# Performance work log

Hardware: AMD Instinct MI355X
Metric: run time of the kernel (lower is better)

## Reference

```python
import jax, jax.numpy as jnp
import numpy as np

B, T, C, D = 8, 4096, 1024, 128  # batch, seq (=block_size), dim_embd, head_features

def setup_inputs() -> dict:
    key = jax.random.key(0)
    k1, k2, k3, k4 = jax.random.split(key, 4)
    s = 0.02
    return {
        "x": jax.random.normal(k1, (B, T, C), dtype=jnp.float32),
        "wq": jax.random.normal(k2, (C, D), dtype=jnp.float32) * s,
        "wk": jax.random.normal(k3, (C, D), dtype=jnp.float32) * s,
        "wv": jax.random.normal(k4, (C, D), dtype=jnp.float32) * s,
    }

def reference(x, wq, wk, wv):
    # q,k,v: [B,T,D]
    q = jnp.einsum('btc,cd->btd', x, wq)
    k = jnp.einsum('btc,cd->btd', x, wk)
    v = jnp.einsum('btc,cd->btd', x, wv)
    scale = k.shape[-1] ** -0.5
    wei = jnp.einsum('bqd,bkd->bqk', q, k) * scale  # [B,T,T]
    causal = jnp.tril(jnp.ones((T, T), dtype=bool))
    wei = jnp.where(causal, wei, -jnp.inf)
    attn = jax.nn.softmax(wei, axis=-1)  # dropout p=0.0 -> identity
    out = jnp.einsum('bqk,bkd->bqd', attn, v)  # [B,T,D]
    return out
```

## Files before the change

### kernel.cpp

```cpp
#include <hip/hip_runtime.h>

#define TT 4096
#define CC 1024
#define DD 128

typedef __attribute__((ext_vector_type(8))) short s16x8;
typedef __attribute__((ext_vector_type(4))) short s16x4;
typedef __attribute__((ext_vector_type(8))) __bf16 bf16x8;
typedef __attribute__((ext_vector_type(4))) float f32x4;

__device__ __forceinline__ short f2bf(float f) {
    union { float f; unsigned u; } v; v.f = f;
    unsigned r = v.u + 0x7fffu + ((v.u >> 16) & 1u);
    return (short)(r >> 16);
}

__device__ __forceinline__ unsigned cvt_pk(float lo, float hi) {
    unsigned r;
    asm("v_cvt_pk_bf16_f32 %0, %1, %2" : "=v"(r) : "v"(lo), "v"(hi));
    return r;
}

__device__ __forceinline__ f32x4 mfma16(s16x8 a, s16x8 b, f32x4 c) {
    return __builtin_amdgcn_mfma_f32_16x16x32_bf16(
        __builtin_bit_cast(bf16x8, a), __builtin_bit_cast(bf16x8, b), c, 0, 0, 0);
}

__device__ __forceinline__ void gload_lds16(const short* g, short* l) {
    __builtin_amdgcn_global_load_lds(
        (const __attribute__((address_space(1))) void*)g,
        (__attribute__((address_space(3))) void*)l, 16, 0, 0);
}

__global__ void wt_kernel(const float* __restrict__ wq, const float* __restrict__ wk,
                          const float* __restrict__ wv, short* __restrict__ wT) {
    int idx = blockIdx.x * 256 + threadIdx.x;
    int d = idx & 127;
    int c = (idx >> 7) & 1023;
    int wsel = idx >> 17;
    const float* w = (wsel == 0) ? wq : (wsel == 1) ? wk : wv;
    float v = w[(size_t)c * DD + d];
    if (wsel == 0) v *= 0.08838834764831845f;
    wT[(size_t)wsel * DD * CC + (size_t)d * CC + c] = f2bf(v);
}

__global__ __launch_bounds__(512)
void qkv_kernel(const float* __restrict__ x, const short* __restrict__ wT,
                short* __restrict__ qo, short* __restrict__ ko, short* __restrict__ vTo) {
    __shared__ short lw[2][384 * 64];
    const int mt = blockIdx.x;
    const int tid = threadIdx.x, lane = tid & 63, wid = tid >> 6;
    const int l15 = lane & 15, g = lane >> 4;
    const int wm = wid >> 1, wn = wid & 1;
    const int arow = mt * 128 + wm * 32 + l15;
    const float* xr0 = x + (size_t)arow * CC + g * 8;
    const float* xr1 = xr0 + (size_t)16 * CC;

    const f32x4 fz = {0.f, 0.f, 0.f, 0.f};
    f32x4 acc[2][12];
#pragma unroll
    for (int mr = 0; mr < 2; mr++)
#pragma unroll
        for (int nr = 0; nr < 12; nr++) acc[mr][nr] = fz;

    const int swr = wid * 48;
    const short* wsrc = wT + (size_t)(swr + (lane >> 3)) * CC + (lane & 7) * 8;

    float4 pa[2][2][2];
#define LOADA(kc) do { \
    _Pragma("unroll") for (int mr_ = 0; mr_ < 2; mr_++) \
    _Pragma("unroll") for (int ks_ = 0; ks_ < 2; ks_++) { \
        const float* p_ = (mr_ ? xr1 : xr0) + (kc) * 64 + ks_ * 32; \
        pa[mr_][ks_][0] = *(const float4*)p_; \
        pa[mr_][ks_][1] = *(const float4*)(p_ + 4); } \
} while (0)
#define STAGEW(kc, buf) do { \
    _Pragma("unroll") for (int j_ = 0; j_ < 6; j_++) \
        gload_lds16(wsrc + (size_t)(j_ * 8) * CC + (kc) * 64, &lw[buf][(swr + j_ * 8) * 64]); \
} while (0)

    LOADA(0);
    STAGEW(0, 0);
    asm volatile("s_waitcnt vmcnt(0)" ::: "memory");
    __builtin_amdgcn_s_barrier();
    int cur = 0;

    for (int kc = 0; kc < 16; kc++) {
        s16x8 af[2][2];
#pragma unroll
        for (int mr = 0; mr < 2; mr++)
#pragma unroll
            for (int ks = 0; ks < 2; ks++) {
                union { unsigned u[4]; s16x8 v; } cv;
                cv.u[0] = cvt_pk(pa[mr][ks][0].x, pa[mr][ks][0].y);
                cv.u[1] = cvt_pk(pa[mr][ks][0].z, pa[mr][ks][0].w);
                cv.u[2] = cvt_pk(pa[mr][ks][1].x, pa[mr][ks][1].y);
                cv.u[3] = cvt_pk(pa[mr][ks][1].z, pa[mr][ks][1].w);
                af[mr][ks] = cv.v;
            }
        if (kc < 15) { LOADA(kc + 1); STAGEW(kc + 1, cur ^ 1); }
        __builtin_amdgcn_s_setprio(1);
#pragma unroll
        for (int ks = 0; ks < 2; ks++)
#pragma unroll
            for (int nr = 0; nr < 12; nr++) {
                const s16x8 bfg = *(const s16x8*)
                    &lw[cur][(wn * 192 + nr * 16 + l15) * 64 + ks * 32 + g * 8];
                acc[0][nr] = mfma16(af[0][ks], bfg, acc[0][nr]);
                acc[1][nr] = mfma16(af[1][ks], bfg, acc[1][nr]);
            }
        __builtin_amdgcn_s_setprio(0);
        asm volatile("s_waitcnt vmcnt(0) lgkmcnt(0)" ::: "memory");
        __builtin_amdgcn_s_barrier();
        cur ^= 1;
    }

    const int bidx = mt >> 5;
    const int tb = (mt & 31) * 128 + wm * 32;
#pragma unroll
    for (int mr = 0; mr < 2; mr++)
#pragma unroll
        for (int nr = 0; nr < 12; nr++) {
            const int n = wn * 192 + nr * 16 + l15;
            if (n < 256) {
                short* dst; int d;
                if (n < 128) { dst = qo; d = n; } else { dst = ko; d = n - 128; }
#pragma unroll
                for (int i = 0; i < 4; i++) {
                    int t = tb + mr * 16 + g * 4 + i;
                    dst[((size_t)bidx * TT + t) * DD + d] = f2bf(acc[mr][nr][i]);
                }
            } else {
                const int d = n - 256;
                const int t = tb + mr * 16 + g * 4;
                uint2 u;
                u.x = cvt_pk(acc[mr][nr][0], acc[mr][nr][1]);
                u.y = cvt_pk(acc[mr][nr][2], acc[mr][nr][3]);
                *(uint2*)(vTo + ((size_t)bidx * DD + d) * TT + t) = u;
            }
        }
}

__device__ __forceinline__ void attn_stage8(const short* kT, const short* vT, int kv0,
                                            short* lkb, short* lvb, int wid, int lane) {
#pragma unroll
    for (int j = 0; j < 2; j++) {
        int rbk = wid * 8 + j * 4;
        int rk = rbk + (lane >> 4);
        int ck = (lane & 15) ^ (rk & 7);
        gload_lds16(kT + (size_t)(kv0 + rk) * DD + ck * 8, lkb + rbk * 128);
        int rbv = wid * 16 + j * 8;
        int dv = rbv + (lane >> 3);
        int cv = (lane & 7) ^ (dv & 7);
        gload_lds16(vT + (size_t)dv * TT + kv0 + cv * 8, lvb + rbv * 64);
    }
}

__global__ __launch_bounds__(512)
void attn_kernel(const short* __restrict__ qb, const short* __restrict__ kb,
                 const short* __restrict__ vb, float* __restrict__ out) {
    __shared__ short lk[2][64 * 128];
    __shared__ short lv[2][128 * 64];
    __shared__ short lp[8 * 16 * 64];
    const int id = blockIdx.x;
    const int b = id & 7;
    const int p = id >> 3;
    const int tid = threadIdx.x, lane = tid & 63, wid = tid >> 6;
    const int l15 = lane & 15, g = lane >> 4;
    const int qt_w = (wid < 4) ? p : 63 - p;
    const int wq0 = qt_w * 64 + (wid & 3) * 16;
    const int tmax = 63 - p;

    s16x8 qf[4];
    {
        const short* qp = qb + ((size_t)b * TT + wq0 + l15) * DD + g * 8;
#pragma unroll
        for (int ks = 0; ks < 4; ks++) qf[ks] = *(const s16x8*)(qp + ks * 32);
    }
    const f32x4 fz = {0.f, 0.f, 0.f, 0.f};
    f32x4 o[8];
#pragma unroll
    for (int n = 0; n < 8; n++) o[n] = fz;
    float rmax = -1e30f, rsum = 0.f;

    const short* kT = kb + (size_t)b * TT * DD;
    const short* vT = vb + (size_t)b * DD * TT;

    attn_stage8(kT, vT, 0, lk[0], lv[0], wid, lane);
    asm volatile("s_waitcnt vmcnt(0)" ::: "memory");
    __builtin_amdgcn_s_barrier();
    int cur = 0;

    for (int t = 0; t <= tmax; t++) {
        if (t < tmax) attn_stage8(kT, vT, (t + 1) * 64, lk[cur ^ 1], lv[cur ^ 1], wid, lane);
        if (t <= qt_w) {
            const int kv0 = t * 64;
            const char* lkc = (const char*)&lk[cur][0];
            const char* lvc = (const char*)&lv[cur][0];

            f32x4 s[4];
            __builtin_amdgcn_s_setprio(1);
#pragma unroll
            for (int sub = 0; sub < 4; sub++) {
                f32x4 a = fz;
#pragma unroll
                for (int ks = 0; ks < 4; ks++) {
                    int row = sub * 16 + l15;
                    int byte = (row * 256 + ks * 64 + g * 16) ^ ((row & 7) << 4);
                    s16x8 kf = *(const s16x8*)(lkc + byte);
                    a = mfma16(kf, qf[ks], a);
                }
                s[sub] = a;
            }
            __builtin_amdgcn_s_setprio(0);
            if (t == qt_w) {
#pragma unroll
                for (int sub = 0; sub < 4; sub++)
#pragma unroll
                    for (int i = 0; i < 4; i++) {
                        int k = kv0 + sub * 16 + 4 * g + i;
                        if (k > wq0 + l15) s[sub][i] = -1e30f;
                    }
            }
            float m0 = s[0][0];
#pragma unroll
            for (int sub = 0; sub < 4; sub++)
#pragma unroll
                for (int i = 0; i < 4; i++) m0 = fmaxf(m0, s[sub][i]);
            m0 = fmaxf(m0, __shfl_xor(m0, 16));
            m0 = fmaxf(m0, __shfl_xor(m0, 32));
            float mnew = fmaxf(rmax, m0);
            float scal = __expf(rmax - mnew);
            rmax = mnew;
            float ls = 0.f;
#pragma unroll
            for (int sub = 0; sub < 4; sub++)
#pragma unroll
                for (int i = 0; i < 4; i++) {
                    float pv = __expf(s[sub][i] - mnew);
                    s[sub][i] = pv;
                    ls += pv;
                }
            ls += __shfl_xor(ls, 16);
            ls += __shfl_xor(ls, 32);
            rsum = rsum * scal + ls;
#pragma unroll
            for (int sub = 0; sub < 4; sub++) {
                uint2 w01;
                w01.x = cvt_pk(s[sub][0], s[sub][1]);
                w01.y = cvt_pk(s[sub][2], s[sub][3]);
                int byte = (l15 * 128 + sub * 32 + g * 8) ^ ((l15 & 7) << 4);
                *(uint2*)((char*)lp + wid * 2048 + byte) = w01;
            }
#pragma unroll
            for (int n = 0; n < 8; n++)
#pragma unroll
                for (int i = 0; i < 4; i++) o[n][i] *= scal;
            __builtin_amdgcn_s_setprio(1);
#pragma unroll
            for (int ks2 = 0; ks2 < 2; ks2++) {
                int pbyte = (l15 * 128 + ks2 * 64 + g * 16) ^ ((l15 & 7) << 4);
                s16x8 pf = *(const s16x8*)((const char*)lp + wid * 2048 + pbyte);
#pragma unroll
                for (int n = 0; n < 8; n++) {
                    int vrow = n * 16 + l15;
                    int vbyte = (vrow * 128 + ks2 * 64 + g * 16) ^ ((vrow & 7) << 4);
                    s16x8 vf = *(const s16x8*)(lvc + vbyte);
                    o[n] = mfma16(vf, pf, o[n]);
                }
            }
            __builtin_amdgcn_s_setprio(0);
        }
        asm volatile("s_waitcnt vmcnt(0) lgkmcnt(0)" ::: "memory");
        __builtin_amdgcn_s_barrier();
        cur ^= 1;
    }
    float inv = 1.0f / rsum;
    float* orow = out + ((size_t)b * TT + wq0 + l15) * DD;
#pragma unroll
    for (int n = 0; n < 8; n++) {
        float4 r;
        r.x = o[n][0] * inv; r.y = o[n][1] * inv;
        r.z = o[n][2] * inv; r.w = o[n][3] * inv;
        *(float4*)(orow + n * 16 + 4 * g) = r;
    }
}

extern "C" void kernel_launch(void* const* d_in, const int* in_sizes, int n_in,
                              void* d_out, int out_size, void* d_ws, size_t ws_size,
                              hipStream_t stream) {
    const float* x  = (const float*)d_in[0];
    const float* wq = (const float*)d_in[1];
    const float* wk = (const float*)d_in[2];
    const float* wv = (const float*)d_in[3];
    float* out = (float*)d_out;
    char* ws = (char*)d_ws;
    short* wT = (short*)ws;
    short* qb = (short*)(ws + 786432);
    short* kb = (short*)(ws + 786432 + 8388608);
    short* vb = (short*)(ws + 786432 + 16777216);

    wt_kernel<<<1536, 256, 0, stream>>>(wq, wk, wv, wT);
    qkv_kernel<<<256, 512, 0, stream>>>(x, wT, qb, kb, vb);
    attn_kernel<<<256, 512, 0, stream>>>(qb, kb, vb, out);
}
```

Baseline: 168.3 us.

## Load K/V tiles directly into registers per wave, drop shared LDS staging

The attention kernel stops staging K and V tiles in double-buffered shared memory with block-wide barriers. Each wave now loads its own K and V fragments straight from global memory into registers, prefetching the next K tile during softmax. Blocks shrink to 256 threads, and each wave handles two 16-row query strips in a balanced pair of phases. This removes the barriers and LDS traffic, but every wave now reads K/V separately, which multiplies global/L2 traffic and raises register pressure.

```diff
diff --git a/kernel.cpp b/kernel.cpp
--- a/kernel.cpp
+++ b/kernel.cpp
@@ -141,62 +141,54 @@
         }
 }
 
-__device__ __forceinline__ void attn_stage8(const short* kT, const short* vT, int kv0,
-                                            short* lkb, short* lvb, int wid, int lane) {
-#pragma unroll
-    for (int j = 0; j < 2; j++) {
-        int rbk = wid * 8 + j * 4;
-        int rk = rbk + (lane >> 4);
-        int ck = (lane & 15) ^ (rk & 7);
-        gload_lds16(kT + (size_t)(kv0 + rk) * DD + ck * 8, lkb + rbk * 128);
-        int rbv = wid * 16 + j * 8;
-        int dv = rbv + (lane >> 3);
-        int cv = (lane & 7) ^ (dv & 7);
-        gload_lds16(vT + (size_t)dv * TT + kv0 + cv * 8, lvb + rbv * 64);
-    }
-}
-
-__global__ __launch_bounds__(512)
+__global__ __launch_bounds__(256)
 void attn_kernel(const short* __restrict__ qb, const short* __restrict__ kb,
                  const short* __restrict__ vb, float* __restrict__ out) {
-    __shared__ short lk[2][64 * 128];
-    __shared__ short lv[2][128 * 64];
-    __shared__ short lp[8 * 16 * 64];
+    __shared__ short lp[4][1024];
     const int id = blockIdx.x;
     const int b = id & 7;
-    const int p = id >> 3;
+    const int pg = id >> 3;
     const int tid = threadIdx.x, lane = tid & 63, wid = tid >> 6;
     const int l15 = lane & 15, g = lane >> 4;
-    const int qt_w = (wid < 4) ? p : 63 - p;
-    const int wq0 = qt_w * 64 + (wid & 3) * 16;
-    const int tmax = 63 - p;
-
-    s16x8 qf[4];
-    {
-        const short* qp = qb + ((size_t)b * TT + wq0 + l15) * DD + g * 8;
-#pragma unroll
-        for (int ks = 0; ks < 4; ks++) qf[ks] = *(const s16x8*)(qp + ks * 32);
-    }
-    const f32x4 fz = {0.f, 0.f, 0.f, 0.f};
-    f32x4 o[8];
-#pragma unroll
-    for (int n = 0; n < 8; n++) o[n] = fz;
-    float rmax = -1e30f, rsum = 0.f;
-
     const short* kT = kb + (size_t)b * TT * DD;
     const short* vT = vb + (size_t)b * DD * TT;
-
-    attn_stage8(kT, vT, 0, lk[0], lv[0], wid, lane);
-    asm volatile("s_waitcnt vmcnt(0)" ::: "memory");
-    __builtin_amdgcn_s_barrier();
-    int cur = 0;
-
-    for (int t = 0; t <= tmax; t++) {
-        if (t < tmax) attn_stage8(kT, vT, (t + 1) * 64, lk[cur ^ 1], lv[cur ^ 1], wid, lane);
-        if (t <= qt_w) {
+    char* lpw = (char*)&lp[wid][0];
+    const f32x4 fz = {0.f, 0.f, 0.f, 0.f};
+
+    for (int ph = 0; ph < 2; ph++) {
+        const int s1 = pg * 4 + wid;
+        const int s = ph ? 255 - s1 : s1;
+        const int tq = s >> 2;
+        const int wq0 = s * 16;
+
+        s16x8 qf[4];
+        {
+            const short* qp = qb + ((size_t)b * TT + wq0 + l15) * DD + g * 8;
+#pragma unroll
+            for (int ks = 0; ks < 4; ks++) qf[ks] = *(const s16x8*)(qp + ks * 32);
+        }
+        f32x4 o[8];
+#pragma unroll
+        for (int n = 0; n < 8; n++) o[n] = fz;
+        float rmax = -1e30f, rsum = 0.f;
+
+        s16x8 kreg[4][4];
+#pragma unroll
+        for (int sub = 0; sub < 4; sub++)
+#pragma unroll
+            for (int ks = 0; ks < 4; ks++)
+                kreg[sub][ks] = *(const s16x8*)
+                    (kT + (size_t)(sub * 16 + l15) * DD + ks * 32 + g * 8);
+
+        for (int t = 0; t <= tq; t++) {
             const int kv0 = t * 64;
-            const char* lkc = (const char*)&lk[cur][0];
-            const char* lvc = (const char*)&lv[cur][0];
+            s16x8 vreg[8][2];
+#pragma unroll
+            for (int n = 0; n < 8; n++)
+#pragma unroll
+                for (int ks2 = 0; ks2 < 2; ks2++)
+                    vreg[n][ks2] = *(const s16x8*)
+                        (vT + (size_t)(n * 16 + l15) * TT + kv0 + ks2 * 32 + g * 8);
 
             f32x4 s[4];
             __builtin_amdgcn_s_setprio(1);
@@ -204,16 +196,12 @@
             for (int sub = 0; sub < 4; sub++) {
                 f32x4 a = fz;
 #pragma unroll
-                for (int ks = 0; ks < 4; ks++) {
-                    int row = sub * 16 + l15;
-                    int byte = (row * 256 + ks * 64 + g * 16) ^ ((row & 7) << 4);
-                    s16x8 kf = *(const s16x8*)(lkc + byte);
-                    a = mfma16(kf, qf[ks], a);
-                }
+                for (int ks = 0; ks < 4; ks++)
+                    a = mfma16(kreg[sub][ks], qf[ks], a);
                 s[sub] = a;
             }
             __builtin_amdgcn_s_setprio(0);
-            if (t == qt_w) {
+            if (t == tq) {
 #pragma unroll
                 for (int sub = 0; sub < 4; sub++)
 #pragma unroll
@@ -244,45 +232,49 @@
             ls += __shfl_xor(ls, 16);
             ls += __shfl_xor(ls, 32);
             rsum = rsum * scal + ls;
+
+            if (t < tq) {
+#pragma unroll
+                for (int sub = 0; sub < 4; sub++)
+#pragma unroll
+                    for (int ks = 0; ks < 4; ks++)
+                        kreg[sub][ks] = *(const s16x8*)
+                            (kT + (size_t)(kv0 + 64 + sub * 16 + l15) * DD + ks * 32 + g * 8);
+            }
+
 #pragma unroll
             for (int sub = 0; sub < 4; sub++) {
                 uint2 w01;
                 w01.x = cvt_pk(s[sub][0], s[sub][1]);
                 w01.y = cvt_pk(s[sub][2], s[sub][3]);
                 int byte = (l15 * 128 + sub * 32 + g * 8) ^ ((l15 & 7) << 4);
-                *(uint2*)((char*)lp + wid * 2048 + byte) = w01;
+                *(uint2*)(lpw + byte) = w01;
             }
 #pragma unroll
             for (int n = 0; n < 8; n++)
 #pragma unroll
                 for (int i = 0; i < 4; i++) o[n][i] *= scal;
+
             __builtin_amdgcn_s_setprio(1);
 #pragma unroll
             for (int ks2 = 0; ks2 < 2; ks2++) {
                 int pbyte = (l15 * 128 + ks2 * 64 + g * 16) ^ ((l15 & 7) << 4);
-                s16x8 pf = *(const s16x8*)((const char*)lp + wid * 2048 + pbyte);
-#pragma unroll
-                for (int n = 0; n < 8; n++) {
-                    int vrow = n * 16 + l15;
-                    int vbyte = (vrow * 128 + ks2 * 64 + g * 16) ^ ((vrow & 7) << 4);
-                    s16x8 vf = *(const s16x8*)(lvc + vbyte);
-                    o[n] = mfma16(vf, pf, o[n]);
-                }
+                s16x8 pf = *(const s16x8*)(lpw + pbyte);
+#pragma unroll
+                for (int n = 0; n < 8; n++)
+                    o[n] = mfma16(vreg[n][ks2], pf, o[n]);
             }
             __builtin_amdgcn_s_setprio(0);
         }
-        asm volatile("s_waitcnt vmcnt(0) lgkmcnt(0)" ::: "memory");
-        __builtin_amdgcn_s_barrier();
-        cur ^= 1;
-    }
-    float inv = 1.0f / rsum;
-    float* orow = out + ((size_t)b * TT + wq0 + l15) * DD;
-#pragma unroll
-    for (int n = 0; n < 8; n++) {
-        float4 r;
-        r.x = o[n][0] * inv; r.y = o[n][1] * inv;
-        r.z = o[n][2] * inv; r.w = o[n][3] * inv;
-        *(float4*)(orow + n * 16 + 4 * g) = r;
+        float inv = 1.0f / rsum;
+        float* orow = out + ((size_t)b * TT + wq0 + l15) * DD;
+#pragma unroll
+        for (int n = 0; n < 8; n++) {
+            float4 r;
+            r.x = o[n][0] * inv; r.y = o[n][1] * inv;
+            r.z = o[n][2] * inv; r.w = o[n][3] * inv;
+            *(float4*)(orow + n * 16 + 4 * g) = r;
+        }
     }
 }
 
@@ -302,5 +294,5 @@
 
     wt_kernel<<<1536, 256, 0, stream>>>(wq, wk, wv, wT);
     qkv_kernel<<<256, 512, 0, stream>>>(x, wT, qb, kb, vb);
-    attn_kernel<<<256, 512, 0, stream>>>(qb, kb, vb, out);
-}
+    attn_kernel<<<256, 256, 0, stream>>>(qb, kb, vb, out);
+}
```

Result: slower. 287.0 us (+70.6%).

## Load K tiles directly into registers with prefetch instead of LDS staging

Applied to the files above, without the earlier changes.

K is no longer staged through shared memory. Each wave loads its own K fragments from global memory straight into registers and prefetches the next tile right after the QK MFMAs. The end-of-iteration wait becomes a partial vmcnt so the K prefetch can stay in flight across the barrier. This removes LDS traffic and bank pressure for K but costs 8x more global/L2 reads of K per block, plus about 64 extra VGPRs that may hurt occupancy.

```diff
diff --git a/kernel.cpp b/kernel.cpp
--- a/kernel.cpp
+++ b/kernel.cpp
@@ -141,14 +141,10 @@
         }
 }
 
-__device__ __forceinline__ void attn_stage8(const short* kT, const short* vT, int kv0,
-                                            short* lkb, short* lvb, int wid, int lane) {
+__device__ __forceinline__ void stage_v(const short* vT, int kv0, short* lvb,
+                                        int wid, int lane) {
 #pragma unroll
     for (int j = 0; j < 2; j++) {
-        int rbk = wid * 8 + j * 4;
-        int rk = rbk + (lane >> 4);
-        int ck = (lane & 15) ^ (rk & 7);
-        gload_lds16(kT + (size_t)(kv0 + rk) * DD + ck * 8, lkb + rbk * 128);
         int rbv = wid * 16 + j * 8;
         int dv = rbv + (lane >> 3);
         int cv = (lane & 7) ^ (dv & 7);
@@ -159,9 +155,8 @@
 __global__ __launch_bounds__(512)
 void attn_kernel(const short* __restrict__ qb, const short* __restrict__ kb,
                  const short* __restrict__ vb, float* __restrict__ out) {
-    __shared__ short lk[2][64 * 128];
     __shared__ short lv[2][128 * 64];
-    __shared__ short lp[8 * 16 * 64];
+    __shared__ short lp[8][1024];
     const int id = blockIdx.x;
     const int b = id & 7;
     const int p = id >> 3;
@@ -170,6 +165,10 @@
     const int qt_w = (wid < 4) ? p : 63 - p;
     const int wq0 = qt_w * 64 + (wid & 3) * 16;
     const int tmax = 63 - p;
+    const short* kT = kb + (size_t)b * TT * DD;
+    const short* vT = vb + (size_t)b * DD * TT;
+    char* lpw = (char*)&lp[wid][0];
+    const f32x4 fz = {0.f, 0.f, 0.f, 0.f};
 
     s16x8 qf[4];
     {
@@ -177,42 +176,42 @@
 #pragma unroll
         for (int ks = 0; ks < 4; ks++) qf[ks] = *(const s16x8*)(qp + ks * 32);
     }
-    const f32x4 fz = {0.f, 0.f, 0.f, 0.f};
     f32x4 o[8];
 #pragma unroll
     for (int n = 0; n < 8; n++) o[n] = fz;
     float rmax = -1e30f, rsum = 0.f;
 
-    const short* kT = kb + (size_t)b * TT * DD;
-    const short* vT = vb + (size_t)b * DD * TT;
-
-    attn_stage8(kT, vT, 0, lk[0], lv[0], wid, lane);
+    s16x8 kreg[4][4];
+#define LOADK(kv0) do { \
+    _Pragma("unroll") for (int sub_ = 0; sub_ < 4; sub_++) \
+    _Pragma("unroll") for (int ks_ = 0; ks_ < 4; ks_++) \
+        kreg[sub_][ks_] = *(const s16x8*) \
+            (kT + (size_t)((kv0) + sub_ * 16 + l15) * DD + ks_ * 32 + g * 8); \
+} while (0)
+
+    LOADK(0);
+    stage_v(vT, 0, lv[0], wid, lane);
     asm volatile("s_waitcnt vmcnt(0)" ::: "memory");
     __builtin_amdgcn_s_barrier();
     int cur = 0;
 
     for (int t = 0; t <= tmax; t++) {
-        if (t < tmax) attn_stage8(kT, vT, (t + 1) * 64, lk[cur ^ 1], lv[cur ^ 1], wid, lane);
+        if (t < tmax) stage_v(vT, (t + 1) * 64, lv[cur ^ 1], wid, lane);
+        asm volatile("" ::: "memory");
         if (t <= qt_w) {
             const int kv0 = t * 64;
-            const char* lkc = (const char*)&lk[cur][0];
-            const char* lvc = (const char*)&lv[cur][0];
-
             f32x4 s[4];
             __builtin_amdgcn_s_setprio(1);
 #pragma unroll
             for (int sub = 0; sub < 4; sub++) {
                 f32x4 a = fz;
 #pragma unroll
-                for (int ks = 0; ks < 4; ks++) {
-                    int row = sub * 16 + l15;
-                    int byte = (row * 256 + ks * 64 + g * 16) ^ ((row & 7) << 4);
-                    s16x8 kf = *(const s16x8*)(lkc + byte);
-                    a = mfma16(kf, qf[ks], a);
-                }
+                for (int ks = 0; ks < 4; ks++)
+                    a = mfma16(kreg[sub][ks], qf[ks], a);
                 s[sub] = a;
             }
             __builtin_amdgcn_s_setprio(0);
+            if (t < qt_w) LOADK((t + 1) * 64);
             if (t == qt_w) {
 #pragma unroll
                 for (int sub = 0; sub < 4; sub++)
@@ -250,7 +249,7 @@
                 w01.x = cvt_pk(s[sub][0], s[sub][1]);
                 w01.y = cvt_pk(s[sub][2], s[sub][3]);
                 int byte = (l15 * 128 + sub * 32 + g * 8) ^ ((l15 & 7) << 4);
-                *(uint2*)((char*)lp + wid * 2048 + byte) = w01;
+                *(uint2*)(lpw + byte) = w01;
             }
 #pragma unroll
             for (int n = 0; n < 8; n++)
@@ -260,18 +259,19 @@
 #pragma unroll
             for (int ks2 = 0; ks2 < 2; ks2++) {
                 int pbyte = (l15 * 128 + ks2 * 64 + g * 16) ^ ((l15 & 7) << 4);
-                s16x8 pf = *(const s16x8*)((const char*)lp + wid * 2048 + pbyte);
+                s16x8 pf = *(const s16x8*)(lpw + pbyte);
 #pragma unroll
                 for (int n = 0; n < 8; n++) {
                     int vrow = n * 16 + l15;
                     int vbyte = (vrow * 128 + ks2 * 64 + g * 16) ^ ((vrow & 7) << 4);
-                    s16x8 vf = *(const s16x8*)(lvc + vbyte);
+                    s16x8 vf = *(const s16x8*)((const char*)&lv[cur][0] + vbyte);
                     o[n] = mfma16(vf, pf, o[n]);
                 }
             }
             __builtin_amdgcn_s_setprio(0);
         }
-        asm volatile("s_waitcnt vmcnt(0) lgkmcnt(0)" ::: "memory");
+        if (t < qt_w) asm volatile("s_waitcnt vmcnt(16)" ::: "memory");
+        else          asm volatile("s_waitcnt vmcnt(0)"  ::: "memory");
         __builtin_amdgcn_s_barrier();
         cur ^= 1;
     }
```

Result: slower. 210.0 us (+24.8%).
